# Kernel optimization log

Hardware: AMD Instinct MI355X
Metric: run time of the kernel (lower is better)

The kernel has to match this reference:

```python
import math
import jax, jax.numpy as jnp
import numpy as np

B, T, C, FD, K, V = 8, 2048, 256, 256, 128, 256

def setup_inputs() -> dict:
    key = jax.random.key(0)
    ks = jax.random.split(key, 8)
    s = 0.02
    return {
        "inp": jax.random.normal(ks[0], (B, T, C), jnp.float32),
        "feature": jax.random.normal(ks[1], (B, T, FD), jnp.float32),
        "Wq": jax.random.normal(ks[2], (C + FD, K), jnp.float32) * s,
        "bq": jnp.zeros((K,), jnp.float32),
        "Wk": jax.random.normal(ks[3], (C, K), jnp.float32) * s,
        "bk": jnp.zeros((K,), jnp.float32),
        "Wv": jax.random.normal(ks[4], (C, V), jnp.float32) * s,
        "bv": jnp.zeros((V,), jnp.float32),
    }

def reference(inp, feature, Wq, bq, Wk, bk, Wv, bv):
    # inp: [B,T,C], feature: [B,T,FD]
    t = inp.shape[1]
    q = jnp.concatenate([inp, feature], axis=-1) @ Wq + bq   # [B,T,K]
    k = inp @ Wk + bk                                        # [B,T,K]
    v = inp @ Wv + bv                                        # [B,T,V]
    # scores[b, j, i] = q_j . k_i ; original masks where i > j (strict upper tri)
    scores = jnp.einsum('bjk,bik->bji', q, k)                # [B,T,T]
    mask = jnp.triu(jnp.ones((t, t), dtype=bool), k=1)       # mask[j,i] = i > j
    scores = jnp.where(mask[None], -jnp.inf, scores) / math.sqrt(K)
    # NOTE: original softmax is over dim=1 (the query/row axis), not the key axis
    attn = jax.nn.softmax(scores, axis=1)                    # [B,T,T]
    out = jnp.einsum('bji,biv->bjv', attn, v)                # [B,T,V]
    return jnp.concatenate([inp, out], axis=-1)              # [B,T,C+V]
```

## Files before the change

### kernel.cpp

```cpp
#include <hip/hip_runtime.h>
#include <hip/hip_bf16.h>
#include <cstdint>

#define Bb  8
#define Tt  2048
#define Cc  256
#define FDd 256
#define Kk  128
#define Vv  256
#define BT  (Bb * Tt)
#define NTRI 136

#define INV_SQRT_K 0.08838834764831845f

typedef __bf16 bf16x8 __attribute__((ext_vector_type(8)));
typedef __bf16 bf16x4 __attribute__((ext_vector_type(4)));
typedef float  f32x4  __attribute__((ext_vector_type(4)));

__device__ __forceinline__ void gload16(const void* g, void* l) {
  __builtin_amdgcn_global_load_lds(
      (const __attribute__((address_space(1))) void*)g,
      (__attribute__((address_space(3))) void*)l, 16, 0, 0);
}

__global__ __launch_bounds__(256) void prep_kernel(
    const float4* __restrict__ inp4, const float4* __restrict__ feat4,
    float4* __restrict__ out4, bf16x4* __restrict__ inpB4,
    bf16x4* __restrict__ featB4)
{
  const int g = blockIdx.x * 256 + threadIdx.x;
  const int row = g >> 6, c = g & 63;
  const float4 x = inp4[g];
  out4[(size_t)row * 128 + c] = x;
  bf16x4 xb; xb[0] = (__bf16)x.x; xb[1] = (__bf16)x.y; xb[2] = (__bf16)x.z; xb[3] = (__bf16)x.w;
  inpB4[g] = xb;
  const float4 f = feat4[g];
  bf16x4 fb; fb[0] = (__bf16)f.x; fb[1] = (__bf16)f.y; fb[2] = (__bf16)f.z; fb[3] = (__bf16)f.w;
  featB4[g] = fb;
}

__global__ __launch_bounds__(256) void wprep_kernel(
    const float* __restrict__ Wq, const float* __restrict__ Wk,
    const float* __restrict__ Wv, __bf16* __restrict__ Wqt,
    __bf16* __restrict__ Wkt, __bf16* __restrict__ Wvt)
{
  const int g = blockIdx.x * 256 + threadIdx.x;
  if (g < 65536) {
    const int n = g >> 9, k = g & 511;
    Wqt[g] = (__bf16)Wq[k * 128 + n];
  } else if (g < 98304) {
    const int h = g - 65536;
    const int n = h >> 8, k = h & 255;
    Wkt[h] = (__bf16)Wk[k * 128 + n];
  } else {
    const int h = g - 98304;
    const int n = h >> 8, k = h & 255;
    Wvt[h] = (__bf16)Wv[k * 256 + n];
  }
}

__global__ __launch_bounds__(256, 3) void qkv_mfma_kernel(
    const __bf16* __restrict__ inpB, const __bf16* __restrict__ featB,
    const __bf16* __restrict__ Wqt, const __bf16* __restrict__ Wkt,
    const __bf16* __restrict__ Wvt,
    const float* __restrict__ bq, const float* __restrict__ bk,
    const float* __restrict__ bv,
    __bf16* __restrict__ qb, __bf16* __restrict__ kb, __bf16* __restrict__ vT)
{
  __shared__ __bf16 Atile[128 * 64];
  __shared__ __bf16 Btile[128 * 64];
  const int panel = blockIdx.y;
  const int m0 = blockIdx.x * 128;
  const int lane = threadIdx.x & 63, wave = threadIdx.x >> 6;
  const int cl = lane & 15, quad = lane >> 4;
  const int jl0 = (wave >> 1) * 64;
  const int vl0 = (wave & 1) * 64;

  const __bf16* Wt; const float* bias; int kblocks;
  if (panel == 0)      { Wt = Wqt; bias = bq; kblocks = 8; }
  else if (panel == 1) { Wt = Wkt; bias = bk; kblocks = 4; }
  else                 { Wt = Wvt + (size_t)(panel - 2) * 128 * 256;
                         bias = bv + (panel - 2) * 128; kblocks = 4; }
  const int Kd = kblocks * 64;

  const int lrow = lane >> 3;
  const int lchunk = ((lane & 7) ^ lrow) * 8;

  f32x4 acc[4][4];
#pragma unroll
  for (int mt = 0; mt < 4; ++mt)
#pragma unroll
    for (int nt = 0; nt < 4; ++nt) acc[mt][nt] = (f32x4){0.f, 0.f, 0.f, 0.f};

  for (int kb = 0; kb < kblocks; ++kb) {
    const __bf16* Asrc = (panel == 0 && kb >= 4) ? featB : inpB;
    const int koff = (panel == 0 && kb >= 4) ? (kb - 4) * 64 : kb * 64;
    __syncthreads();
#pragma unroll
    for (int t = 0; t < 4; ++t) {
      const int r0 = wave * 32 + t * 8;
      gload16(Asrc + (size_t)(m0 + r0 + lrow) * 256 + koff + lchunk, Atile + r0 * 64);
      gload16(Wt + (size_t)(r0 + lrow) * Kd + kb * 64 + lchunk, Btile + r0 * 64);
    }
    __syncthreads();
#pragma unroll
    for (int ks = 0; ks < 2; ++ks) {
      bf16x8 af[4], bfr[4];
#pragma unroll
      for (int mt = 0; mt < 4; ++mt) {
        const int jlr = jl0 + mt * 16 + cl;
        af[mt] = *(const bf16x8*)(Atile + jlr * 64 + (((ks * 4 + quad) ^ (jlr & 7)) * 8));
      }
#pragma unroll
      for (int nt = 0; nt < 4; ++nt) {
        const int vlr = vl0 + nt * 16 + cl;
        bfr[nt] = *(const bf16x8*)(Btile + vlr * 64 + (((ks * 4 + quad) ^ (vlr & 7)) * 8));
      }
#pragma unroll
      for (int mt = 0; mt < 4; ++mt)
#pragma unroll
        for (int nt = 0; nt < 4; ++nt)
          acc[mt][nt] = __builtin_amdgcn_mfma_f32_16x16x32_bf16(af[mt], bfr[nt], acc[mt][nt], 0, 0, 0);
    }
  }

  if (panel < 2) {
    __bf16* dst = (panel == 0) ? qb : kb;
    const float scale = (panel == 0) ? INV_SQRT_K : 1.0f;
#pragma unroll
    for (int mt = 0; mt < 4; ++mt) {
      const int row = m0 + jl0 + mt * 16 + quad * 4;
#pragma unroll
      for (int nt = 0; nt < 4; ++nt) {
        const int col = vl0 + nt * 16 + cl;
        const float bs = bias[col];
#pragma unroll
        for (int r = 0; r < 4; ++r)
          dst[(size_t)(row + r) * Kk + col] = (__bf16)((acc[mt][nt][r] + bs) * scale);
      }
    }
  } else {
    const int b = m0 >> 11;
#pragma unroll
    for (int mt = 0; mt < 4; ++mt) {
      const int t0 = (m0 & (Tt - 1)) + jl0 + mt * 16 + quad * 4;
#pragma unroll
      for (int nt = 0; nt < 4; ++nt) {
        const int vcol = (panel - 2) * 128 + vl0 + nt * 16 + cl;
        const float bs = bias[vl0 + nt * 16 + cl];
        bf16x4 v4;
#pragma unroll
        for (int r = 0; r < 4; ++r) v4[r] = (__bf16)(acc[mt][nt][r] + bs);
        *(bf16x4*)(vT + (size_t)(b * Vv + vcol) * Tt + t0) = v4;
      }
    }
  }
}

__global__ __launch_bounds__(256) void sexp_kernel(
    const __bf16* __restrict__ qb, const __bf16* __restrict__ kb,
    __bf16* __restrict__ expS, float* __restrict__ partialD)
{
  const int b = blockIdx.y, l = blockIdx.x;
  int jt = 0, base = 0;
  while (base + jt + 1 <= l) { base += jt + 1; ++jt; }
  const int it = l - base;

  const int lane = threadIdx.x & 63, wave = threadIdx.x >> 6;
  const int cl = lane & 15, quad = lane >> 4;
  const int j0 = jt * 128 + (wave >> 1) * 64;
  const int i0 = it * 128 + (wave & 1) * 64;
  const size_t rowbase = (size_t)b * Tt;

  bf16x8 af[4][4], bfr[4][4];
  const __bf16* qrow = qb + (rowbase + j0 + cl) * Kk + quad * 8;
  const __bf16* krow = kb + (rowbase + i0 + cl) * Kk + quad * 8;
#pragma unroll
  for (int mt = 0; mt < 4; ++mt)
#pragma unroll
    for (int ks = 0; ks < 4; ++ks) af[mt][ks] = *(const bf16x8*)(qrow + mt * 16 * Kk + ks * 32);
#pragma unroll
  for (int nt = 0; nt < 4; ++nt)
#pragma unroll
    for (int ks = 0; ks < 4; ++ks) bfr[nt][ks] = *(const bf16x8*)(krow + nt * 16 * Kk + ks * 32);

  f32x4 acc[4][4];
#pragma unroll
  for (int mt = 0; mt < 4; ++mt)
#pragma unroll
    for (int nt = 0; nt < 4; ++nt) acc[mt][nt] = (f32x4){0.f, 0.f, 0.f, 0.f};

#pragma unroll
  for (int ks = 0; ks < 4; ++ks)
#pragma unroll
    for (int mt = 0; mt < 4; ++mt)
#pragma unroll
      for (int nt = 0; nt < 4; ++nt)
        acc[mt][nt] = __builtin_amdgcn_mfma_f32_16x16x32_bf16(af[mt][ks], bfr[nt][ks], acc[mt][nt], 0, 0, 0);

  __bf16* slot = expS + ((size_t)(b * NTRI + l)) * (128 * 128);
  const bool diag = (it == jt);
  float cs[4] = {0.f, 0.f, 0.f, 0.f};
#pragma unroll
  for (int mt = 0; mt < 4; ++mt) {
    const int jl = (wave >> 1) * 64 + mt * 16 + quad * 4;
#pragma unroll
    for (int nt = 0; nt < 4; ++nt) {
      const int il = (wave & 1) * 64 + nt * 16 + cl;
#pragma unroll
      for (int r = 0; r < 4; ++r) {
        float p = __expf(acc[mt][nt][r]);
        if (diag && (i0 + nt * 16 + cl) > (j0 + mt * 16 + quad * 4 + r)) p = 0.f;
        const __bf16 pb = (__bf16)p;
        cs[nt] += (float)pb;
        slot[(size_t)(jl + r) * 128 + il] = pb;
      }
    }
  }
  __shared__ float lcs[4][64];
#pragma unroll
  for (int nt = 0; nt < 4; ++nt) {
    cs[nt] += __shfl_xor(cs[nt], 16);
    cs[nt] += __shfl_xor(cs[nt], 32);
  }
  if (quad == 0) {
#pragma unroll
    for (int nt = 0; nt < 4; ++nt) lcs[wave][nt * 16 + cl] = cs[nt];
  }
  __syncthreads();
  const int tid = threadIdx.x;
  if (tid < 128) {
    const int w0 = (tid < 64) ? 0 : 1;
    const int lc = tid & 63;
    const float s = lcs[w0][lc] + lcs[w0 + 2][lc];
    partialD[((size_t)b * 16 + jt) * Tt + it * 128 + tid] = s;
  }
}

__global__ __launch_bounds__(256) void dreduce_kernel(
    const float* __restrict__ partialD, float* __restrict__ recipD)
{
  const int g = blockIdx.x * 256 + threadIdx.x;
  const int b = g >> 11, i = g & (Tt - 1);
  float s = 0.f;
#pragma unroll
  for (int jt = 0; jt < 16; ++jt) s += partialD[((size_t)b * 16 + jt) * Tt + i];
  recipD[g] = 1.0f / s;
}

__global__ __launch_bounds__(256) void vscale_kernel(
    bf16x8* __restrict__ vT8, const float* __restrict__ recipD)
{
  const int g = blockIdx.x * 256 + threadIdx.x;
  const size_t e0 = (size_t)g * 8;
  const int i = (int)(e0 & (Tt - 1));
  const int b = (int)(e0 >> 19);
  bf16x8 v = vT8[g];
  const f32x4 r0 = *(const f32x4*)(recipD + (size_t)b * Tt + i);
  const f32x4 r1 = *(const f32x4*)(recipD + (size_t)b * Tt + i + 4);
#pragma unroll
  for (int t = 0; t < 4; ++t) v[t] = (__bf16)((float)v[t] * r0[t]);
#pragma unroll
  for (int t = 0; t < 4; ++t) v[4 + t] = (__bf16)((float)v[4 + t] * r1[t]);
  vT8[g] = v;
}

__global__ __launch_bounds__(256, 3) void pvgemm_kernel(
    const __bf16* __restrict__ expS, const __bf16* __restrict__ vT,
    float* __restrict__ out)
{
  __shared__ __bf16 Atile[128 * 64];
  __shared__ __bf16 Btile[128 * 64];
  const int b = blockIdx.y;
  const int jt = 15 - (blockIdx.x >> 1);
  const int nh = blockIdx.x & 1;
  const int lane = threadIdx.x & 63, wave = threadIdx.x >> 6;
  const int cl = lane & 15, quad = lane >> 4;
  const int jl0 = (wave >> 1) * 64;
  const int vl0 = (wave & 1) * 64;

  const int kblocks = (jt + 1) * 2;
  const size_t slotbase = (size_t)(b * NTRI + (jt * (jt + 1)) / 2) * 16384;
  const __bf16* vbase = vT + ((size_t)b * Vv + nh * 128) * Tt;

  const int lrow = lane >> 3;
  const int lchunk = ((lane & 7) ^ lrow) * 8;

  f32x4 acc[4][4];
#pragma unroll
  for (int mt = 0; mt < 4; ++mt)
#pragma unroll
    for (int nt = 0; nt < 4; ++nt) acc[mt][nt] = (f32x4){0.f, 0.f, 0.f, 0.f};

  for (int kb = 0; kb < kblocks; ++kb) {
    const int i0 = kb * 64;
    const __bf16* Ag = expS + slotbase + (size_t)(kb >> 1) * 16384 + (kb & 1) * 64;
    __syncthreads();
#pragma unroll
    for (int t = 0; t < 4; ++t) {
      const int r0 = wave * 32 + t * 8;
      gload16(Ag + (size_t)(r0 + lrow) * 128 + lchunk, Atile + r0 * 64);
      gload16(vbase + (size_t)(r0 + lrow) * Tt + i0 + lchunk, Btile + r0 * 64);
    }
    __syncthreads();
#pragma unroll
    for (int ks = 0; ks < 2; ++ks) {
      bf16x8 af[4], bfr[4];
#pragma unroll
      for (int mt = 0; mt < 4; ++mt) {
        const int jlr = jl0 + mt * 16 + cl;
        af[mt] = *(const bf16x8*)(Atile + jlr * 64 + (((ks * 4 + quad) ^ (jlr & 7)) * 8));
      }
#pragma unroll
      for (int nt = 0; nt < 4; ++nt) {
        const int vlr = vl0 + nt * 16 + cl;
        bfr[nt] = *(const bf16x8*)(Btile + vlr * 64 + (((ks * 4 + quad) ^ (vlr & 7)) * 8));
      }
#pragma unroll
      for (int mt = 0; mt < 4; ++mt)
#pragma unroll
        for (int nt = 0; nt < 4; ++nt)
          acc[mt][nt] = __builtin_amdgcn_mfma_f32_16x16x32_bf16(af[mt], bfr[nt], acc[mt][nt], 0, 0, 0);
    }
  }

  float* orow = out + ((size_t)b * Tt + jt * 128 + jl0) * (size_t)(Cc + Vv)
              + Cc + nh * 128 + vl0;
#pragma unroll
  for (int mt = 0; mt < 4; ++mt)
#pragma unroll
    for (int nt = 0; nt < 4; ++nt)
#pragma unroll
      for (int r = 0; r < 4; ++r)
        orow[(size_t)(mt * 16 + quad * 4 + r) * (Cc + Vv) + nt * 16 + cl] = acc[mt][nt][r];
}

extern "C" void kernel_launch(void* const* d_in, const int* in_sizes, int n_in,
                              void* d_out, int out_size, void* d_ws, size_t ws_size,
                              hipStream_t stream) {
  const float* inp  = (const float*)d_in[0];
  const float* feat = (const float*)d_in[1];
  const float* Wq   = (const float*)d_in[2];
  const float* bq   = (const float*)d_in[3];
  const float* Wk   = (const float*)d_in[4];
  const float* bk   = (const float*)d_in[5];
  const float* Wv   = (const float*)d_in[6];
  const float* bv   = (const float*)d_in[7];
  float* out = (float*)d_out;

  char* ws = (char*)d_ws;
  __bf16* inpB   = (__bf16*)(ws);
  __bf16* featB  = (__bf16*)(ws + (8u << 20));
  __bf16* qb     = (__bf16*)(ws + (16u << 20));
  __bf16* kb     = (__bf16*)(ws + (20u << 20));
  __bf16* vT     = (__bf16*)(ws + (24u << 20));
  __bf16* Wqt    = (__bf16*)(ws + (32u << 20));
  __bf16* Wkt    = (__bf16*)(ws + (32u << 20) + (128u << 10));
  __bf16* Wvt    = (__bf16*)(ws + (32u << 20) + (192u << 10));
  float*  partialD = (float*)(ws + (33u << 20));
  float*  recipD   = (float*)(ws + (35u << 20));
  __bf16* expS     = (__bf16*)(ws + (36u << 20));

  prep_kernel<<<dim3(BT * 64 / 256), 256, 0, stream>>>(
      (const float4*)inp, (const float4*)feat, (float4*)out,
      (bf16x4*)inpB, (bf16x4*)featB);
  wprep_kernel<<<dim3(640), 256, 0, stream>>>(Wq, Wk, Wv, Wqt, Wkt, Wvt);
  qkv_mfma_kernel<<<dim3(BT / 128, 4), 256, 0, stream>>>(
      inpB, featB, Wqt, Wkt, Wvt, bq, bk, bv, qb, kb, vT);
  sexp_kernel<<<dim3(NTRI, Bb), 256, 0, stream>>>(qb, kb, expS, partialD);
  dreduce_kernel<<<dim3(BT / 256), 256, 0, stream>>>(partialD, recipD);
  vscale_kernel<<<dim3(2048), 256, 0, stream>>>((bf16x8*)vT, recipD);
  pvgemm_kernel<<<dim3(32, Bb), 256, 0, stream>>>(expS, vT, out);
}
```

Before: 182.0 us.

## Stage Q/K tiles in LDS and coalesce exp-score stores via shared memory

The score-exp kernel now loads its Q and K tiles into LDS with async global-to-LDS loads in an XOR-swizzled layout, instead of per-lane strided global reads. The exponentiated scores go to an LDS staging buffer, and are then written to global memory as 16-byte row-contiguous bf16x8 stores instead of scattered 2-byte stores. Launch bounds now ask for two blocks per CU. The change adds about 64KB of LDS per block and extra barriers, which may limit occupancy.

```diff
diff --git a/kernel.cpp b/kernel.cpp
--- a/kernel.cpp
+++ b/kernel.cpp
@@ -157,10 +157,16 @@
   }
 }
 
-__global__ __launch_bounds__(256) void sexp_kernel(
+__global__ __launch_bounds__(256, 2) void sexp_kernel(
     const __bf16* __restrict__ qb, const __bf16* __restrict__ kb,
     __bf16* __restrict__ expS, float* __restrict__ partialD)
 {
+  __shared__ __bf16 tiles[2 * 128 * 128];
+  __shared__ float lcs[4][64];
+  __bf16* Qtile = tiles;
+  __bf16* Ktile = tiles + 128 * 128;
+  float*  P     = (float*)tiles;
+
   const int b = blockIdx.y, l = blockIdx.x;
   int jt = 0, base = 0;
   while (base + jt + 1 <= l) { base += jt + 1; ++jt; }
@@ -168,56 +174,70 @@
 
   const int lane = threadIdx.x & 63, wave = threadIdx.x >> 6;
   const int cl = lane & 15, quad = lane >> 4;
-  const int j0 = jt * 128 + (wave >> 1) * 64;
-  const int i0 = it * 128 + (wave & 1) * 64;
+  const int jl0 = (wave >> 1) * 64;
+  const int il0 = (wave & 1) * 64;
   const size_t rowbase = (size_t)b * Tt;
 
-  bf16x8 af[4][4], bfr[4][4];
-  const __bf16* qrow = qb + (rowbase + j0 + cl) * Kk + quad * 8;
-  const __bf16* krow = kb + (rowbase + i0 + cl) * Kk + quad * 8;
+  {
+    const int srow = lane >> 4;
+    const int cslot = lane & 15;
+    const __bf16* qsrc = qb + (rowbase + jt * 128) * Kk;
+    const __bf16* ksrc = kb + (rowbase + it * 128) * Kk;
+#pragma unroll
+    for (int t = 0; t < 8; ++t) {
+      const int r0 = wave * 32 + t * 4;
+      const int row = r0 + srow;
+      const int cg = (cslot ^ (row & 7)) * 8;
+      gload16(qsrc + (size_t)row * Kk + cg, Qtile + r0 * 128);
+      gload16(ksrc + (size_t)row * Kk + cg, Ktile + r0 * 128);
+    }
+  }
+  __syncthreads();
+
+  f32x4 acc[4][4];
 #pragma unroll
   for (int mt = 0; mt < 4; ++mt)
 #pragma unroll
-    for (int ks = 0; ks < 4; ++ks) af[mt][ks] = *(const bf16x8*)(qrow + mt * 16 * Kk + ks * 32);
-#pragma unroll
-  for (int nt = 0; nt < 4; ++nt)
-#pragma unroll
-    for (int ks = 0; ks < 4; ++ks) bfr[nt][ks] = *(const bf16x8*)(krow + nt * 16 * Kk + ks * 32);
-
-  f32x4 acc[4][4];
-#pragma unroll
-  for (int mt = 0; mt < 4; ++mt)
-#pragma unroll
     for (int nt = 0; nt < 4; ++nt) acc[mt][nt] = (f32x4){0.f, 0.f, 0.f, 0.f};
 
 #pragma unroll
-  for (int ks = 0; ks < 4; ++ks)
+  for (int s = 0; s < 4; ++s) {
+    bf16x8 af[4], bfr[4];
+#pragma unroll
+    for (int mt = 0; mt < 4; ++mt) {
+      const int jlr = jl0 + mt * 16 + cl;
+      af[mt] = *(const bf16x8*)(Qtile + jlr * 128 + (((s * 4 + quad) ^ (jlr & 7)) * 8));
+    }
+#pragma unroll
+    for (int nt = 0; nt < 4; ++nt) {
+      const int ilr = il0 + nt * 16 + cl;
+      bfr[nt] = *(const bf16x8*)(Ktile + ilr * 128 + (((s * 4 + quad) ^ (ilr & 7)) * 8));
+    }
 #pragma unroll
     for (int mt = 0; mt < 4; ++mt)
 #pragma unroll
       for (int nt = 0; nt < 4; ++nt)
-        acc[mt][nt] = __builtin_amdgcn_mfma_f32_16x16x32_bf16(af[mt][ks], bfr[nt][ks], acc[mt][nt], 0, 0, 0);
-
-  __bf16* slot = expS + ((size_t)(b * NTRI + l)) * (128 * 128);
+        acc[mt][nt] = __builtin_amdgcn_mfma_f32_16x16x32_bf16(af[mt], bfr[nt], acc[mt][nt], 0, 0, 0);
+  }
+  __syncthreads();
+
   const bool diag = (it == jt);
   float cs[4] = {0.f, 0.f, 0.f, 0.f};
 #pragma unroll
   for (int mt = 0; mt < 4; ++mt) {
-    const int jl = (wave >> 1) * 64 + mt * 16 + quad * 4;
+    const int jl = jl0 + mt * 16 + quad * 4;
 #pragma unroll
     for (int nt = 0; nt < 4; ++nt) {
-      const int il = (wave & 1) * 64 + nt * 16 + cl;
+      const int il = il0 + nt * 16 + cl;
 #pragma unroll
       for (int r = 0; r < 4; ++r) {
         float p = __expf(acc[mt][nt][r]);
-        if (diag && (i0 + nt * 16 + cl) > (j0 + mt * 16 + quad * 4 + r)) p = 0.f;
-        const __bf16 pb = (__bf16)p;
-        cs[nt] += (float)pb;
-        slot[(size_t)(jl + r) * 128 + il] = pb;
-      }
-    }
-  }
-  __shared__ float lcs[4][64];
+        if (diag && il > (jl + r)) p = 0.f;
+        cs[nt] += (float)(__bf16)p;
+        P[(jl + r) * 128 + il] = p;
+      }
+    }
+  }
 #pragma unroll
   for (int nt = 0; nt < 4; ++nt) {
     cs[nt] += __shfl_xor(cs[nt], 16);
@@ -228,6 +248,23 @@
     for (int nt = 0; nt < 4; ++nt) lcs[wave][nt * 16 + cl] = cs[nt];
   }
   __syncthreads();
+
+  __bf16* slot = expS + ((size_t)(b * NTRI + l)) * (128 * 128);
+  {
+    const int srow = lane >> 4;
+    const int c0 = (lane & 15) * 8;
+#pragma unroll
+    for (int t = 0; t < 8; ++t) {
+      const int row = wave * 32 + t * 4 + srow;
+      const f32x4 p0 = *(const f32x4*)(P + row * 128 + c0);
+      const f32x4 p1 = *(const f32x4*)(P + row * 128 + c0 + 4);
+      bf16x8 pb;
+#pragma unroll
+      for (int u = 0; u < 4; ++u) { pb[u] = (__bf16)p0[u]; pb[4 + u] = (__bf16)p1[u]; }
+      *(bf16x8*)(slot + (size_t)row * 128 + c0) = pb;
+    }
+  }
+
   const int tid = threadIdx.x;
   if (tid < 128) {
     const int w0 = (tid < 64) ? 0 : 1;
```

After: 174.4 us. 1.04x faster.
